# Kernel optimization log

Measured on AMD Instinct MI355X. Metric: run time of the kernel, lower is better.

Reference implementation:

```python
import jax, jax.numpy as jnp
import numpy as np

B, T, C, H = 4, 2048, 1024, 16
D = C // H  # head_size = 64

def setup_inputs() -> dict:
    key = jax.random.key(0)
    ks = jax.random.split(key, 9)
    s = 1.0 / np.sqrt(C)
    return {
        "x":  jax.random.normal(ks[0], (B, T, C), dtype=jnp.float32),
        "Wq": jax.random.normal(ks[1], (C, C), dtype=jnp.float32) * s,
        "bq": jnp.zeros((C,), dtype=jnp.float32),
        "Wk": jax.random.normal(ks[2], (C, C), dtype=jnp.float32) * s,
        "bk": jnp.zeros((C,), dtype=jnp.float32),
        "Wv": jax.random.normal(ks[3], (C, C), dtype=jnp.float32) * s,
        "bv": jnp.zeros((C,), dtype=jnp.float32),
        "Wp": jax.random.normal(ks[4], (C, C), dtype=jnp.float32) * s,
        "bp": jnp.zeros((C,), dtype=jnp.float32),
    }

def reference(x, Wq, bq, Wk, bk, Wv, bv, Wp, bp):
    # projections -> [B, H, T, D]
    def split_heads(y):
        return y.reshape(B, T, H, D).transpose(0, 2, 1, 3)
    q = split_heads(x @ Wq + bq)
    k = split_heads(x @ Wk + bk)
    v = split_heads(x @ Wv + bv)
    scale = 1.0 / np.sqrt(D)
    att = jnp.einsum('bhqd,bhkd->bhqk', q, k) * scale  # [B,H,T,T]
    causal = jnp.tril(jnp.ones((T, T), dtype=bool))
    att = jnp.where(causal, att, -jnp.inf)
    att = jax.nn.softmax(att, axis=-1)
    # dropout p=0.0 (eval): identity
    y = jnp.einsum('bhqk,bhkd->bhqd', att, v)  # [B,H,T,D]
    y = y.transpose(0, 2, 1, 3).reshape(B, T, C)
    return y @ Wp + bp
```

## Files before the change

kernel.cpp:

```cpp
#include <hip/hip_runtime.h>
#include <hip/hip_bf16.h>

#define B_ 4
#define T_ 2048
#define C_ 1024
#define H_ 16
#define D_ 64
#define M_ (B_*T_)

typedef __bf16 bf16x8 __attribute__((ext_vector_type(8)));
typedef float  f32x4  __attribute__((ext_vector_type(4)));
typedef float  f32x16 __attribute__((ext_vector_type(16)));

__device__ __forceinline__ unsigned short f2bf(float f) {
  unsigned u = __builtin_bit_cast(unsigned, f);
  u += 0x7FFF + ((u >> 16) & 1);
  return (unsigned short)(u >> 16);
}

__device__ __forceinline__ float exp2fast(float x) {
#if __has_builtin(__builtin_amdgcn_exp2f)
  return __builtin_amdgcn_exp2f(x);
#else
  float r; asm("v_exp_f32 %0, %1" : "=v"(r) : "v"(x)); return r;
#endif
}

__device__ __forceinline__ void gload_lds16(const void* g, void* l) {
  __builtin_amdgcn_global_load_lds(
      (const __attribute__((address_space(1))) void*)g,
      (__attribute__((address_space(3))) void*)l, 16, 0, 0);
}

__global__ void cvt_f32_bf16(const float* __restrict__ in,
                             unsigned short* __restrict__ out, int n4) {
  int i = blockIdx.x * blockDim.x + threadIdx.x;
  if (i < n4) {
    float4 v = ((const float4*)in)[i];
    ushort4 o;
    o.x = f2bf(v.x); o.y = f2bf(v.y); o.z = f2bf(v.z); o.w = f2bf(v.w);
    ((ushort4*)out)[i] = o;
  }
}

__global__ void transpose_cvt(const float* __restrict__ w0, const float* __restrict__ w1,
                              const float* __restrict__ w2, const float* __restrict__ w3,
                              unsigned short* __restrict__ tqkv,
                              unsigned short* __restrict__ tp) {
  __shared__ float tile[32][33];
  const float* src; unsigned short* dst;
  switch (blockIdx.z) {
    case 0: src = w0; dst = tqkv; break;
    case 1: src = w1; dst = tqkv + (size_t)C_ * C_; break;
    case 2: src = w2; dst = tqkv + (size_t)2 * C_ * C_; break;
    default: src = w3; dst = tp; break;
  }
  int bx = blockIdx.x * 32;
  int by = blockIdx.y * 32;
  int tx = threadIdx.x, ty = threadIdx.y;
  #pragma unroll
  for (int j = 0; j < 4; ++j)
    tile[ty + 8*j][tx] = src[(size_t)(by + ty + 8*j) * C_ + bx + tx];
  __syncthreads();
  #pragma unroll
  for (int j = 0; j < 4; ++j)
    dst[(size_t)(bx + ty + 8*j) * C_ + by + tx] = f2bf(tile[tx][ty + 8*j]);
}

__global__ __launch_bounds__(256, 2)
void gemm_qkv(const unsigned short* __restrict__ A,
              const unsigned short* __restrict__ Bt,
              const float* __restrict__ bq, const float* __restrict__ bk,
              const float* __restrict__ bv,
              unsigned short* __restrict__ qout, unsigned short* __restrict__ kout,
              unsigned short* __restrict__ vout, float qscale)
{
  __shared__ unsigned short ls[2 * 128 * 64];
  unsigned short* lsA = ls;
  unsigned short* lsB = ls + 128 * 64;
  const int wave = threadIdx.x >> 6;
  const int lane = threadIdx.x & 63;
  const int rowBase = blockIdx.y * 128;
  const int colBase = blockIdx.x * 128;
  const int rowOff = (wave >> 1) * 64;
  const int colOff = (wave & 1) * 64;
  const int lr = lane & 15;
  const int lg = lane >> 4;

  f32x4 acc[4][4] = {};

  const int chunkRow = lane >> 3;
  const int srcColE  = (((lane & 7) ^ (lane >> 3)) * 8);

  for (int k0 = 0; k0 < C_; k0 += 64) {
    #pragma unroll
    for (int c = 0; c < 4; ++c) {
      int chunk = c * 4 + wave;
      int r = chunk * 8 + chunkRow;
      gload_lds16(A  + (size_t)(rowBase + r) * C_ + k0 + srcColE, &lsA[chunk * 512]);
      gload_lds16(Bt + (size_t)(colBase + r) * C_ + k0 + srcColE, &lsB[chunk * 512]);
    }
    __syncthreads();
    #pragma unroll
    for (int kk = 0; kk < 2; ++kk) {
      bf16x8 af[4], bfr[4];
      const int kbyte = (kk * 32 + lg * 8) * 2;
      #pragma unroll
      for (int m = 0; m < 4; ++m) {
        int row = rowOff + m * 16 + lr;
        af[m] = *(const bf16x8*)((const char*)lsA + row * 128 + (kbyte ^ ((row & 7) << 4)));
      }
      #pragma unroll
      for (int n = 0; n < 4; ++n) {
        int row = colOff + n * 16 + lr;
        bfr[n] = *(const bf16x8*)((const char*)lsB + row * 128 + (kbyte ^ ((row & 7) << 4)));
      }
      #pragma unroll
      for (int m = 0; m < 4; ++m)
        #pragma unroll
        for (int n = 0; n < 4; ++n)
          acc[m][n] = __builtin_amdgcn_mfma_f32_16x16x32_bf16(af[m], bfr[n], acc[m][n], 0, 0, 0);
    }
    __syncthreads();
  }

  const int mid = colBase >> 10;
  const float* bias = (mid == 0) ? bq : (mid == 1) ? bk : bv;
  const float oscale = (mid == 0) ? qscale : 1.f;
  unsigned short* outp = (mid == 0) ? qout : (mid == 1) ? kout : vout;

  char* rpb = (char*)(ls + wave * 4096);
  const int colW = colBase + colOff;
  const int h  = (colW & 1023) >> 6;
  const int b  = (rowBase + rowOff) >> 11;
  const int tb = (rowBase + rowOff) & 2047;

  #pragma unroll
  for (int m = 0; m < 4; ++m)
    #pragma unroll
    for (int n = 0; n < 4; ++n) {
      int colL = n * 16 + lr;
      float bs = bias[(colW + colL) & 1023];
      #pragma unroll
      for (int j = 0; j < 4; ++j) {
        int rowL = m * 16 + lg * 4 + j;
        unsigned short v = f2bf((acc[m][n][j] + bs) * oscale);
        int wr, wc;
        if (mid == 2) {
          int t2 = (rowL & ~12) | ((rowL & 4) << 1) | ((rowL & 8) >> 1);
          wr = colL; wc = t2;
        } else {
          wr = rowL; wc = colL;
        }
        *(unsigned short*)(rpb + wr * 128 + ((wc * 2) ^ ((wr & 7) << 4))) = v;
      }
    }

  const int rb = lane >> 3;
  const int g  = lane & 7;
  if (mid == 2) {
    unsigned short* ob = outp + (((size_t)b * H_ + h) * D_) * T_ + tb;
    #pragma unroll
    for (int p = 0; p < 8; ++p) {
      int d = rb + p * 8;
      bf16x8 v = *(const bf16x8*)(rpb + d * 128 + ((g * 16) ^ ((d & 7) << 4)));
      *(bf16x8*)(ob + (size_t)d * T_ + g * 8) = v;
    }
  } else {
    unsigned short* ob = outp + (((size_t)b * H_ + h) * T_ + tb) * D_;
    #pragma unroll
    for (int p = 0; p < 8; ++p) {
      int r = rb + p * 8;
      bf16x8 v = *(const bf16x8*)(rpb + r * 128 + ((g * 16) ^ ((r & 7) << 4)));
      *(bf16x8*)(ob + (size_t)r * D_ + g * 8) = v;
    }
  }
}

__global__ __launch_bounds__(256, 2)
void gemm_proj(const unsigned short* __restrict__ A,
               const unsigned short* __restrict__ Bt,
               const float* __restrict__ bias,
               float* __restrict__ Cout)
{
  __shared__ unsigned short lsA[128 * 64];
  __shared__ unsigned short lsB[128 * 64];
  const int wave = threadIdx.x >> 6;
  const int lane = threadIdx.x & 63;
  const int rowBase = blockIdx.y * 128;
  const int colBase = blockIdx.x * 128;
  const int rowOff = (wave >> 1) * 64;
  const int colOff = (wave & 1) * 64;
  const int lr = lane & 15;
  const int lg = lane >> 4;

  f32x4 acc[4][4] = {};

  const int chunkRow = lane >> 3;
  const int srcColE  = (((lane & 7) ^ (lane >> 3)) * 8);

  for (int k0 = 0; k0 < C_; k0 += 64) {
    #pragma unroll
    for (int c = 0; c < 4; ++c) {
      int chunk = c * 4 + wave;
      int r = chunk * 8 + chunkRow;
      gload_lds16(A  + (size_t)(rowBase + r) * C_ + k0 + srcColE, &lsA[chunk * 512]);
      gload_lds16(Bt + (size_t)(colBase + r) * C_ + k0 + srcColE, &lsB[chunk * 512]);
    }
    __syncthreads();
    #pragma unroll
    for (int kk = 0; kk < 2; ++kk) {
      bf16x8 af[4], bfr[4];
      const int kbyte = (kk * 32 + lg * 8) * 2;
      #pragma unroll
      for (int m = 0; m < 4; ++m) {
        int row = rowOff + m * 16 + lr;
        af[m] = *(const bf16x8*)((const char*)lsA + row * 128 + (kbyte ^ ((row & 7) << 4)));
      }
      #pragma unroll
      for (int n = 0; n < 4; ++n) {
        int row = colOff + n * 16 + lr;
        bfr[n] = *(const bf16x8*)((const char*)lsB + row * 128 + (kbyte ^ ((row & 7) << 4)));
      }
      #pragma unroll
      for (int m = 0; m < 4; ++m)
        #pragma unroll
        for (int n = 0; n < 4; ++n)
          acc[m][n] = __builtin_amdgcn_mfma_f32_16x16x32_bf16(af[m], bfr[n], acc[m][n], 0, 0, 0);
    }
    __syncthreads();
  }

  #pragma unroll
  for (int m = 0; m < 4; ++m) {
    int row0 = rowBase + rowOff + m * 16 + lg * 4;
    #pragma unroll
    for (int n = 0; n < 4; ++n) {
      int col = colBase + colOff + n * 16 + lr;
      float bs = bias[col];
      #pragma unroll
      for (int j = 0; j < 4; ++j)
        Cout[(size_t)(row0 + j) * C_ + col] = acc[m][n][j] + bs;
    }
  }
}

__global__ __launch_bounds__(256, 2)
void attn12(const unsigned short* __restrict__ q,
            const unsigned short* __restrict__ k,
            const unsigned short* __restrict__ vp,
            unsigned short* __restrict__ y)
{
  __shared__ unsigned short lsK[3][64 * 64];
  __shared__ unsigned short lsV[2][64 * 64];
  const int tid  = threadIdx.x;
  const int wave = tid >> 6;
  const int lane = tid & 63;
  const int col  = lane & 31;
  const int hi   = lane >> 5;

  const int bid = blockIdx.x;
  const int xcd = bid & 7;
  const int idx = bid >> 3;
  const int bh  = xcd * 8 + (idx & 7);
  const int ss  = 15 - (idx >> 3);
  const int b = bh >> 4, h = bh & 15;

  const unsigned short* qh = q  + (size_t)bh * T_ * D_;
  const unsigned short* kh = k  + (size_t)bh * T_ * D_;
  const unsigned short* vh = vp + (size_t)bh * D_ * T_;

  const int srow = tid >> 3;
  const int srcE = ((tid & 7) * 8) ^ ((srow & 7) << 3);
  const unsigned short* ksrc = kh + srow * D_ + srcE;
  const unsigned short* vsrc = vh + srow * T_ + srcE;

  const int swz = (col & 7) << 4;
  const f32x16 zc = {};

  const int q0 = ss * 128 + wave * 32;
  const int nsteps = 2 * ss + 2;

  bf16x8 bqf[4];
  {
    const unsigned short* qrow = qh + (size_t)(q0 + col) * D_ + hi * 8;
    #pragma unroll
    for (int ks = 0; ks < 4; ++ks) bqf[ks] = *(const bf16x8*)(qrow + ks * 16);
  }

  f32x16 ot0 = {}, ot1 = {};
  float m = -INFINITY, l = 0.f;
  bf16x8 pf0, pf1, pf2, pf3;

  auto STAGEK = [&](int t) {
    unsigned short* bK = &lsK[0][0] + (t % 3) * 4096;
    const unsigned short* kg = ksrc + (size_t)t * 64 * D_;
    gload_lds16(kg,           bK + tid * 8);
    gload_lds16(kg + 32 * D_, bK + (tid + 256) * 8);
  };
  auto STAGEV = [&](int t) {
    unsigned short* bV = &lsV[0][0] + (t & 1) * 4096;
    const unsigned short* vg = vsrc + t * 64;
    gload_lds16(vg,           bV + tid * 8);
    gload_lds16(vg + 32 * T_, bV + (tid + 256) * 8);
  };

  STAGEK(0);
  STAGEV(0);
  STAGEK(1);

  for (int s = 0; s < nsteps; ++s) {
    if (s + 1 < nsteps) {
      asm volatile("s_waitcnt vmcnt(2)" ::: "memory");
    } else {
      asm volatile("s_waitcnt vmcnt(0)" ::: "memory");
    }
    __builtin_amdgcn_s_barrier();
    __builtin_amdgcn_sched_barrier(0);
    if (s + 1 < nsteps) STAGEV(s + 1);
    if (s + 2 < nsteps) STAGEK(s + 2);

    const int n0 = s * 64;
    if (n0 <= q0 + 31) {
      const bool two = (n0 < q0);
      const unsigned short* baseK = &lsK[0][0] + (s % 3) * 4096;
      const unsigned short* baseV = &lsV[0][0] + (s & 1) * 4096;
      f32x16 st0, st1;
      {
        const char* kb0 = (const char*)baseK + col * 128;
        __builtin_amdgcn_s_setprio(1);
        st0 = __builtin_amdgcn_mfma_f32_32x32x16_bf16(
                *(const bf16x8*)(kb0 + ((0 * 32 + hi * 16) ^ swz)), bqf[0], zc, 0, 0, 0);
        st0 = __builtin_amdgcn_mfma_f32_32x32x16_bf16(
                *(const bf16x8*)(kb0 + ((1 * 32 + hi * 16) ^ swz)), bqf[1], st0, 0, 0, 0);
        st0 = __builtin_amdgcn_mfma_f32_32x32x16_bf16(
                *(const bf16x8*)(kb0 + ((2 * 32 + hi * 16) ^ swz)), bqf[2], st0, 0, 0, 0);
        st0 = __builtin_amdgcn_mfma_f32_32x32x16_bf16(
                *(const bf16x8*)(kb0 + ((3 * 32 + hi * 16) ^ swz)), bqf[3], st0, 0, 0, 0);
        if (two) {
          const char* kb1 = kb0 + 32 * 128;
          f32x16 a;
          a = __builtin_amdgcn_mfma_f32_32x32x16_bf16(
                *(const bf16x8*)(kb1 + ((0 * 32 + hi * 16) ^ swz)), bqf[0], zc, 0, 0, 0);
          a = __builtin_amdgcn_mfma_f32_32x32x16_bf16(
                *(const bf16x8*)(kb1 + ((1 * 32 + hi * 16) ^ swz)), bqf[1], a, 0, 0, 0);
          a = __builtin_amdgcn_mfma_f32_32x32x16_bf16(
                *(const bf16x8*)(kb1 + ((2 * 32 + hi * 16) ^ swz)), bqf[2], a, 0, 0, 0);
          a = __builtin_amdgcn_mfma_f32_32x32x16_bf16(
                *(const bf16x8*)(kb1 + ((3 * 32 + hi * 16) ^ swz)), bqf[3], a, 0, 0, 0);
          st1 = a;
        }
        __builtin_amdgcn_s_setprio(0);
      }
      if (n0 + 63 > q0) {
        #pragma unroll
        for (int rr = 0; rr < 16; ++rr) {
          int key0 = n0 + (rr & 3) + 8 * (rr >> 2) + 4 * hi;
          if (key0 > q0 + col) st0[rr] = -INFINITY;
          if (two) { if (key0 + 32 > q0 + col) st1[rr] = -INFINITY; }
        }
      }
      float mm;
      {
        float a0 = fmaxf(fmaxf(st0[0], st0[1]), fmaxf(st0[2], st0[3]));
        float a1 = fmaxf(fmaxf(st0[4], st0[5]), fmaxf(st0[6], st0[7]));
        float a2 = fmaxf(fmaxf(st0[8], st0[9]), fmaxf(st0[10], st0[11]));
        float a3 = fmaxf(fmaxf(st0[12], st0[13]), fmaxf(st0[14], st0[15]));
        if (two) {
          a0 = fmaxf(a0, fmaxf(fmaxf(st1[0], st1[1]), fmaxf(st1[2], st1[3])));
          a1 = fmaxf(a1, fmaxf(fmaxf(st1[4], st1[5]), fmaxf(st1[6], st1[7])));
          a2 = fmaxf(a2, fmaxf(fmaxf(st1[8], st1[9]), fmaxf(st1[10], st1[11])));
          a3 = fmaxf(a3, fmaxf(fmaxf(st1[12], st1[13]), fmaxf(st1[14], st1[15])));
        }
        mm = fmaxf(fmaxf(a0, a1), fmaxf(a2, a3));
      }
      if (!__all(mm <= m + 8.f)) {
        float mf = fmaxf(mm, __shfl_xor(mm, 32));
        float mnew = fmaxf(m, mf);
        float corr = exp2fast(m - mnew);
        m = mnew;
        l *= corr;
        #pragma unroll
        for (int rr = 0; rr < 16; ++rr) { ot0[rr] *= corr; ot1[rr] *= corr; }
      }
      {
        float pa[8];
        bf16x8 w;
        #pragma unroll
        for (int e = 0; e < 8; ++e) { pa[e] = exp2fast(st0[e] - m); w[e] = (__bf16)pa[e]; }
        pf0 = w;
        l += ((pa[0] + pa[1]) + (pa[2] + pa[3])) + ((pa[4] + pa[5]) + (pa[6] + pa[7]));
      }
      {
        float pb[8];
        bf16x8 w;
        #pragma unroll
        for (int e = 0; e < 8; ++e) { pb[e] = exp2fast(st0[8 + e] - m); w[e] = (__bf16)pb[e]; }
        pf1 = w;
        l += ((pb[0] + pb[1]) + (pb[2] + pb[3])) + ((pb[4] + pb[5]) + (pb[6] + pb[7]));
      }
      if (two) {
        float pa[8];
        bf16x8 w;
        #pragma unroll
        for (int e = 0; e < 8; ++e) { pa[e] = exp2fast(st1[e] - m); w[e] = (__bf16)pa[e]; }
        pf2 = w;
        l += ((pa[0] + pa[1]) + (pa[2] + pa[3])) + ((pa[4] + pa[5]) + (pa[6] + pa[7]));
        float pb[8];
        #pragma unroll
        for (int e = 0; e < 8; ++e) { pb[e] = exp2fast(st1[8 + e] - m); w[e] = (__bf16)pb[e]; }
        pf3 = w;
        l += ((pb[0] + pb[1]) + (pb[2] + pb[3])) + ((pb[4] + pb[5]) + (pb[6] + pb[7]));
      }
      {
        const char* vb0 = (const char*)baseV + col * 128;
        const char* vb1 = vb0 + 32 * 128;
        __builtin_amdgcn_s_setprio(1);
        #pragma unroll
        for (int ks = 0; ks < 2; ++ks) {
          bf16x8 pw = ks ? pf1 : pf0;
          bf16x8 av0 = *(const bf16x8*)(vb0 + ((ks * 32 + hi * 16) ^ swz));
          bf16x8 av1 = *(const bf16x8*)(vb1 + ((ks * 32 + hi * 16) ^ swz));
          ot0 = __builtin_amdgcn_mfma_f32_32x32x16_bf16(av0, pw, ot0, 0, 0, 0);
          ot1 = __builtin_amdgcn_mfma_f32_32x32x16_bf16(av1, pw, ot1, 0, 0, 0);
        }
        if (two) {
          #pragma unroll
          for (int ks = 2; ks < 4; ++ks) {
            bf16x8 pw = (ks == 3) ? pf3 : pf2;
            bf16x8 av0 = *(const bf16x8*)(vb0 + ((ks * 32 + hi * 16) ^ swz));
            bf16x8 av1 = *(const bf16x8*)(vb1 + ((ks * 32 + hi * 16) ^ swz));
            ot0 = __builtin_amdgcn_mfma_f32_32x32x16_bf16(av0, pw, ot0, 0, 0, 0);
            ot1 = __builtin_amdgcn_mfma_f32_32x32x16_bf16(av1, pw, ot1, 0, 0, 0);
          }
        }
        __builtin_amdgcn_s_setprio(0);
      }
    }
    __builtin_amdgcn_sched_barrier(0);
  }

  float lf = l + __shfl_xor(l, 32);
  float inv = 1.f / lf;
  unsigned short* yrow = y + ((size_t)b * T_ + q0 + col) * C_ + h * D_;
  #pragma unroll
  for (int a = 0; a < 4; ++a) {
    ushort4 o4;
    o4.x = f2bf(ot0[4 * a + 0] * inv);
    o4.y = f2bf(ot0[4 * a + 1] * inv);
    o4.z = f2bf(ot0[4 * a + 2] * inv);
    o4.w = f2bf(ot0[4 * a + 3] * inv);
    *(ushort4*)(yrow + 8 * a + 4 * hi) = o4;
  }
  #pragma unroll
  for (int a = 0; a < 4; ++a) {
    ushort4 o4;
    o4.x = f2bf(ot1[4 * a + 0] * inv);
    o4.y = f2bf(ot1[4 * a + 1] * inv);
    o4.z = f2bf(ot1[4 * a + 2] * inv);
    o4.w = f2bf(ot1[4 * a + 3] * inv);
    *(ushort4*)(yrow + 32 + 8 * a + 4 * hi) = o4;
  }
}

extern "C" void kernel_launch(void* const* d_in, const int* in_sizes, int n_in,
                              void* d_out, int out_size, void* d_ws, size_t ws_size,
                              hipStream_t stream) {
  const float* x  = (const float*)d_in[0];
  const float* Wq = (const float*)d_in[1];
  const float* bq = (const float*)d_in[2];
  const float* Wk = (const float*)d_in[3];
  const float* bk = (const float*)d_in[4];
  const float* Wv = (const float*)d_in[5];
  const float* bv = (const float*)d_in[6];
  const float* Wp = (const float*)d_in[7];
  const float* bp = (const float*)d_in[8];
  float* out = (float*)d_out;

  char* ws = (char*)d_ws;
  unsigned short* xb    = (unsigned short*)ws; ws += (size_t)M_ * C_ * 2;
  unsigned short* wqkvt = (unsigned short*)ws; ws += (size_t)3 * C_ * C_ * 2;
  unsigned short* wpt   = (unsigned short*)ws; ws += (size_t)C_ * C_ * 2;
  unsigned short* qb    = (unsigned short*)ws; ws += (size_t)M_ * C_ * 2;
  unsigned short* kb    = (unsigned short*)ws; ws += (size_t)M_ * C_ * 2;
  unsigned short* vtb   = (unsigned short*)ws; ws += (size_t)M_ * C_ * 2;
  unsigned short* yb    = (unsigned short*)ws; ws += (size_t)M_ * C_ * 2;

  cvt_f32_bf16<<<dim3((M_ * C_ / 4 + 255) / 256), dim3(256), 0, stream>>>(x, xb, M_ * C_ / 4);
  transpose_cvt<<<dim3(32, 32, 4), dim3(32, 8), 0, stream>>>(Wq, Wk, Wv, Wp, wqkvt, wpt);

  const float qscale = 0.125f * 1.4426950408889634f;
  gemm_qkv<<<dim3(3 * C_ / 128, M_ / 128), dim3(256), 0, stream>>>(
      xb, wqkvt, bq, bk, bv, qb, kb, vtb, qscale);

  attn12<<<dim3(1024), dim3(256), 0, stream>>>(qb, kb, vtb, yb);

  gemm_proj<<<dim3(C_ / 128, M_ / 128), dim3(256), 0, stream>>>(yb, wpt, bp, out);
}
```

Measured before the change: 158.2 us.

## Merge prep kernels, compute softmax row sum via MFMA, use max3 reductions

The x conversion and weight transpose-convert kernels are merged into one launch, with extra z-slices handling the x cast, to save a kernel launch. In attention, the per-lane softmax denominator adds are replaced by MFMAs against a ones vector that accumulate row sums on the matrix unit. The max reduction is regrouped into three-input max operations. The MFMA row sum accumulates bf16-rounded probabilities rather than the fp32 values and adds matrix-unit work, in exchange for fewer VALU adds and the final cross-lane shuffle.

```diff
diff --git a/kernel.cpp b/kernel.cpp
--- a/kernel.cpp
+++ b/kernel.cpp
@@ -26,30 +26,35 @@
 #endif
 }
 
+__device__ __forceinline__ float max3f(float a, float b, float c) {
+  return fmaxf(fmaxf(a, b), c);
+}
+
 __device__ __forceinline__ void gload_lds16(const void* g, void* l) {
   __builtin_amdgcn_global_load_lds(
       (const __attribute__((address_space(1))) void*)g,
       (__attribute__((address_space(3))) void*)l, 16, 0, 0);
 }
 
-__global__ void cvt_f32_bf16(const float* __restrict__ in,
-                             unsigned short* __restrict__ out, int n4) {
-  int i = blockIdx.x * blockDim.x + threadIdx.x;
-  if (i < n4) {
-    float4 v = ((const float4*)in)[i];
+__global__ void prep(const float* __restrict__ x,
+                     const float* __restrict__ w0, const float* __restrict__ w1,
+                     const float* __restrict__ w2, const float* __restrict__ w3,
+                     unsigned short* __restrict__ xb,
+                     unsigned short* __restrict__ tqkv,
+                     unsigned short* __restrict__ tp) {
+  __shared__ float tile[32][33];
+  const int z = blockIdx.z;
+  if (z >= 4) {
+    int tid = threadIdx.y * 32 + threadIdx.x;
+    int i = (((z - 4) * 1024) + (blockIdx.y * 32 + blockIdx.x)) * 256 + tid;
+    float4 v = ((const float4*)x)[i];
     ushort4 o;
     o.x = f2bf(v.x); o.y = f2bf(v.y); o.z = f2bf(v.z); o.w = f2bf(v.w);
-    ((ushort4*)out)[i] = o;
-  }
-}
-
-__global__ void transpose_cvt(const float* __restrict__ w0, const float* __restrict__ w1,
-                              const float* __restrict__ w2, const float* __restrict__ w3,
-                              unsigned short* __restrict__ tqkv,
-                              unsigned short* __restrict__ tp) {
-  __shared__ float tile[32][33];
+    ((ushort4*)xb)[i] = o;
+    return;
+  }
   const float* src; unsigned short* dst;
-  switch (blockIdx.z) {
+  switch (z) {
     case 0: src = w0; dst = tqkv; break;
     case 1: src = w1; dst = tqkv + (size_t)C_ * C_; break;
     case 2: src = w2; dst = tqkv + (size_t)2 * C_ * C_; break;
@@ -278,6 +283,10 @@
   const int swz = (col & 7) << 4;
   const f32x16 zc = {};
 
+  bf16x8 ones;
+  #pragma unroll
+  for (int e = 0; e < 8; ++e) ones[e] = (__bf16)1.0f;
+
   const int q0 = ss * 128 + wave * 32;
   const int nsteps = 2 * ss + 2;
 
@@ -288,8 +297,8 @@
     for (int ks = 0; ks < 4; ++ks) bqf[ks] = *(const bf16x8*)(qrow + ks * 16);
   }
 
-  f32x16 ot0 = {}, ot1 = {};
-  float m = -INFINITY, l = 0.f;
+  f32x16 ot0 = {}, ot1 = {}, lacc = {};
+  float m = -INFINITY;
   bf16x8 pf0, pf1, pf2, pf3;
 
   auto STAGEK = [&](int t) {
@@ -362,60 +371,58 @@
       }
       float mm;
       {
-        float a0 = fmaxf(fmaxf(st0[0], st0[1]), fmaxf(st0[2], st0[3]));
-        float a1 = fmaxf(fmaxf(st0[4], st0[5]), fmaxf(st0[6], st0[7]));
-        float a2 = fmaxf(fmaxf(st0[8], st0[9]), fmaxf(st0[10], st0[11]));
-        float a3 = fmaxf(fmaxf(st0[12], st0[13]), fmaxf(st0[14], st0[15]));
+        float g0 = max3f(st0[0],  st0[1],  st0[2]);
+        float g1 = max3f(st0[3],  st0[4],  st0[5]);
+        float g2 = max3f(st0[6],  st0[7],  st0[8]);
+        float g3 = max3f(st0[9],  st0[10], st0[11]);
+        float g4 = max3f(st0[12], st0[13], st0[14]);
+        mm = fmaxf(max3f(g0, g1, g2), max3f(g3, g4, st0[15]));
         if (two) {
-          a0 = fmaxf(a0, fmaxf(fmaxf(st1[0], st1[1]), fmaxf(st1[2], st1[3])));
-          a1 = fmaxf(a1, fmaxf(fmaxf(st1[4], st1[5]), fmaxf(st1[6], st1[7])));
-          a2 = fmaxf(a2, fmaxf(fmaxf(st1[8], st1[9]), fmaxf(st1[10], st1[11])));
-          a3 = fmaxf(a3, fmaxf(fmaxf(st1[12], st1[13]), fmaxf(st1[14], st1[15])));
+          float h0 = max3f(st1[0],  st1[1],  st1[2]);
+          float h1 = max3f(st1[3],  st1[4],  st1[5]);
+          float h2 = max3f(st1[6],  st1[7],  st1[8]);
+          float h3 = max3f(st1[9],  st1[10], st1[11]);
+          float h4 = max3f(st1[12], st1[13], st1[14]);
+          mm = fmaxf(mm, fmaxf(max3f(h0, h1, h2), max3f(h3, h4, st1[15])));
         }
-        mm = fmaxf(fmaxf(a0, a1), fmaxf(a2, a3));
       }
       if (!__all(mm <= m + 8.f)) {
         float mf = fmaxf(mm, __shfl_xor(mm, 32));
         float mnew = fmaxf(m, mf);
         float corr = exp2fast(m - mnew);
         m = mnew;
-        l *= corr;
+        lacc[0] *= corr;
         #pragma unroll
         for (int rr = 0; rr < 16; ++rr) { ot0[rr] *= corr; ot1[rr] *= corr; }
       }
       {
-        float pa[8];
         bf16x8 w;
         #pragma unroll
-        for (int e = 0; e < 8; ++e) { pa[e] = exp2fast(st0[e] - m); w[e] = (__bf16)pa[e]; }
+        for (int e = 0; e < 8; ++e) w[e] = (__bf16)exp2fast(st0[e] - m);
         pf0 = w;
-        l += ((pa[0] + pa[1]) + (pa[2] + pa[3])) + ((pa[4] + pa[5]) + (pa[6] + pa[7]));
       }
       {
-        float pb[8];
         bf16x8 w;
         #pragma unroll
-        for (int e = 0; e < 8; ++e) { pb[e] = exp2fast(st0[8 + e] - m); w[e] = (__bf16)pb[e]; }
+        for (int e = 0; e < 8; ++e) w[e] = (__bf16)exp2fast(st0[8 + e] - m);
         pf1 = w;
-        l += ((pb[0] + pb[1]) + (pb[2] + pb[3])) + ((pb[4] + pb[5]) + (pb[6] + pb[7]));
       }
       if (two) {
-        float pa[8];
         bf16x8 w;
         #pragma unroll
-        for (int e = 0; e < 8; ++e) { pa[e] = exp2fast(st1[e] - m); w[e] = (__bf16)pa[e]; }
+        for (int e = 0; e < 8; ++e) w[e] = (__bf16)exp2fast(st1[e] - m);
         pf2 = w;
-        l += ((pa[0] + pa[1]) + (pa[2] + pa[3])) + ((pa[4] + pa[5]) + (pa[6] + pa[7]));
-        float pb[8];
-        #pragma unroll
-        for (int e = 0; e < 8; ++e) { pb[e] = exp2fast(st1[8 + e] - m); w[e] = (__bf16)pb[e]; }
-        pf3 = w;
-        l += ((pb[0] + pb[1]) + (pb[2] + pb[3])) + ((pb[4] + pb[5]) + (pb[6] + pb[7]));
+        bf16x8 w2;
+        #pragma unroll
+        for (int e = 0; e < 8; ++e) w2[e] = (__bf16)exp2fast(st1[8 + e] - m);
+        pf3 = w2;
       }
       {
         const char* vb0 = (const char*)baseV + col * 128;
         const char* vb1 = vb0 + 32 * 128;
         __builtin_amdgcn_s_setprio(1);
+        lacc = __builtin_amdgcn_mfma_f32_32x32x16_bf16(ones, pf0, lacc, 0, 0, 0);
+        lacc = __builtin_amdgcn_mfma_f32_32x32x16_bf16(ones, pf1, lacc, 0, 0, 0);
         #pragma unroll
         for (int ks = 0; ks < 2; ++ks) {
           bf16x8 pw = ks ? pf1 : pf0;
@@ -425,6 +432,8 @@
           ot1 = __builtin_amdgcn_mfma_f32_32x32x16_bf16(av1, pw, ot1, 0, 0, 0);
         }
         if (two) {
+          lacc = __builtin_amdgcn_mfma_f32_32x32x16_bf16(ones, pf2, lacc, 0, 0, 0);
+          lacc = __builtin_amdgcn_mfma_f32_32x32x16_bf16(ones, pf3, lacc, 0, 0, 0);
           #pragma unroll
           for (int ks = 2; ks < 4; ++ks) {
             bf16x8 pw = (ks == 3) ? pf3 : pf2;
@@ -440,8 +449,7 @@
     __builtin_amdgcn_sched_barrier(0);
   }
 
-  float lf = l + __shfl_xor(l, 32);
-  float inv = 1.f / lf;
+  float inv = 1.f / lacc[0];
   unsigned short* yrow = y + ((size_t)b * T_ + q0 + col) * C_ + h * D_;
   #pragma unroll
   for (int a = 0; a < 4; ++a) {
@@ -486,8 +494,7 @@
   unsigned short* vtb   = (unsigned short*)ws; ws += (size_t)M_ * C_ * 2;
   unsigned short* yb    = (unsigned short*)ws; ws += (size_t)M_ * C_ * 2;
 
-  cvt_f32_bf16<<<dim3((M_ * C_ / 4 + 255) / 256), dim3(256), 0, stream>>>(x, xb, M_ * C_ / 4);
-  transpose_cvt<<<dim3(32, 32, 4), dim3(32, 8), 0, stream>>>(Wq, Wk, Wv, Wp, wqkvt, wpt);
+  prep<<<dim3(32, 32, 12), dim3(32, 8), 0, stream>>>(x, Wq, Wk, Wv, Wp, xb, wqkvt, wpt);
 
   const float qscale = 0.125f * 1.4426950408889634f;
   gemm_qkv<<<dim3(3 * C_ / 128, M_ / 128), dim3(256), 0, stream>>>(
```

Result: faster. 154.8 us (median of 2 runs) (-2.1%).
